# Optimization experiments

Measured on AMD Instinct MI355X. Metric: run time of the kernel, lower is better.

Reference implementation:

```python
import math
import jax, jax.numpy as jnp
import numpy as np


def setup_inputs() -> dict:
    key = jax.random.key(0)
    k1, k2 = jax.random.split(key)
    N, C, K = 1024, 4096, 16384
    x = jax.random.normal(k1, (N, C), dtype=jnp.float32)
    # xavier_normal for (C, K): std = sqrt(2/(C+K))
    w_std = math.sqrt(2.0 / (C + K))
    weights = jax.random.normal(k2, (C, K), dtype=jnp.float32) * w_std
    std = jnp.float32(10.0)
    return {"x": x, "weights": weights, "std": std}


def reference(x, weights, std):
    # x: (N, C); weights: (C, K)
    N, C = x.shape
    K = weights.shape[1]
    side = int(math.sqrt(K))

    # Squared distances ||w_k - x_n||^2 via expansion (same math as
    # norm(weights[None] - x[..., None], dim=1)**2, without the (N,C,K) tensor)
    x2 = jnp.sum(x * x, axis=1, keepdims=True)            # (N, 1)
    w2 = jnp.sum(weights * weights, axis=0)[None, :]       # (1, K)
    xw = jnp.einsum('nc,ck->nk', x, weights)               # (N, K) GEMM
    norms2 = jnp.maximum(x2 + w2 - 2.0 * xw, 0.0)          # (N, K)

    # Best matching unit (detached in original)
    bmu = jnp.argmin(norms2, axis=-1)                      # (N,) int

    # 2D radial basis over the side x side grid, centered at BMU
    row = (bmu // side).astype(jnp.float32)
    col = (bmu % side).astype(jnp.float32)
    t = jnp.arange(side, dtype=jnp.float32)
    gi, gj = jnp.meshgrid(t, t, indexing='ij')
    grid = jnp.stack([gi.reshape(-1), gj.reshape(-1)], axis=-1)  # (K, 2)
    pt = jnp.stack([row, col], axis=-1)[:, None, :]              # (N, 1, 2)
    d2 = jnp.sum((grid[None] - pt) ** 2, axis=-1)                # (N, K)
    phi = jnp.exp(-0.5 * d2 / (std ** 2))
    phi = phi / jnp.sum(phi, axis=-1, keepdims=True)

    return norms2 * phi
```

## Files before the change

### kernel.cpp

```cpp
#include <hip/hip_runtime.h>
#include <stdint.h>

#define NROWS 1024
#define CDIM  4096
#define KDIM  16384
#define SIDE  128

typedef __attribute__((ext_vector_type(8))) short short8;
typedef __attribute__((ext_vector_type(4))) float f32x4;

static __device__ __forceinline__ unsigned short f2bf(float f) {
  unsigned u = __float_as_uint(f);
  u += 0x7fffu + ((u >> 16) & 1u);
  return (unsigned short)(u >> 16);
}
static __device__ __forceinline__ float bf2f(unsigned short h) {
  return __uint_as_float(((unsigned)h) << 16);
}

#define GLOAD_LDS16(g, l)                                                     \
  __builtin_amdgcn_global_load_lds(                                           \
      (const __attribute__((address_space(1))) void*)(g),                     \
      (__attribute__((address_space(3))) void*)(l), 16, 0, 0)

#define SWZ(o) ((o) ^ (((o) >> 3) & 0x70))

__global__ void k_zero(float* __restrict__ w2) {
  w2[blockIdx.x * 256 + threadIdx.x] = 0.f;
}

__global__ __launch_bounds__(256) void k_wconv(const float* __restrict__ w,
                                               unsigned short* __restrict__ whT,
                                               unsigned short* __restrict__ wlT,
                                               float* __restrict__ w2) {
  __shared__ float T[64][65];
  const int k0 = blockIdx.x * 64, c0 = blockIdx.y * 64;
  const int t = threadIdx.x;
#pragma unroll
  for (int i = 0; i < 4; i++) {
    int e = i * 1024 + t * 4;
    int cr = e >> 6, kc = e & 63;
    float4 v = *(const float4*)(w + (size_t)(c0 + cr) * KDIM + k0 + kc);
    T[cr][kc] = v.x; T[cr][kc + 1] = v.y; T[cr][kc + 2] = v.z; T[cr][kc + 3] = v.w;
  }
  __syncthreads();
#pragma unroll
  for (int i = 0; i < 4; i++) {
    int e = i * 1024 + t * 4;
    int kr = e >> 6, cc = e & 63;
    ushort4 hv, lv;
    float f0 = T[cc + 0][kr], f1 = T[cc + 1][kr];
    float f2 = T[cc + 2][kr], f3 = T[cc + 3][kr];
    hv.x = f2bf(f0); lv.x = f2bf(f0 - bf2f(hv.x));
    hv.y = f2bf(f1); lv.y = f2bf(f1 - bf2f(hv.y));
    hv.z = f2bf(f2); lv.z = f2bf(f2 - bf2f(hv.z));
    hv.w = f2bf(f3); lv.w = f2bf(f3 - bf2f(hv.w));
    size_t off = (size_t)(k0 + kr) * CDIM + c0 + cc;
    *(ushort4*)(whT + off) = hv;
    *(ushort4*)(wlT + off) = lv;
    float s = f0 * f0 + f1 * f1 + f2 * f2 + f3 * f3;
#pragma unroll
    for (int off2 = 8; off2 > 0; off2 >>= 1) s += __shfl_down(s, off2);
    if ((t & 15) == 0) atomicAdd(&w2[k0 + kr], s);
  }
}

__global__ __launch_bounds__(256) void k_xconv(const float* __restrict__ x,
                                               unsigned short* __restrict__ xh) {
  size_t i = ((size_t)blockIdx.x * 256 + threadIdx.x) * 4;
  float4 v = *(const float4*)(x + i);
  ushort4 hv;
  hv.x = f2bf(v.x); hv.y = f2bf(v.y); hv.z = f2bf(v.z); hv.w = f2bf(v.w);
  *(ushort4*)(xh + i) = hv;
}

__global__ void k_x2(const float* __restrict__ x, float* __restrict__ x2) {
  const int n = blockIdx.x, l = threadIdx.x;
  const float* row = x + (size_t)n * CDIM;
  float s = 0.f;
#pragma unroll 4
  for (int i = 0; i < 16; i++) {
    float4 v = *(const float4*)(row + (i * 64 + l) * 4);
    s += v.x * v.x + v.y * v.y + v.z * v.z + v.w * v.w;
  }
#pragma unroll
  for (int off = 32; off > 0; off >>= 1) s += __shfl_down(s, off);
  if (l == 0) x2[n] = s;
}

__global__ __launch_bounds__(512, 2) void k_gemm(
    const unsigned short* __restrict__ xh,
    const unsigned short* __restrict__ whT,
    const float* __restrict__ x2, const float* __restrict__ w2,
    float* __restrict__ out) {
  extern __shared__ char smem[];
  const int t = threadIdx.x;
  const int b = blockIdx.x;
  const int L = (b & 7) * 32 + (b >> 3);
  const int m0 = (L & 3) * 256, n0 = (L >> 2) * 256;
  const int lane = t & 63, wid = t >> 6;
  const int wrow = (wid >> 2) * 128;
  const int wcol = (wid & 3) * 64;

  int rowS[4], cbS[4];
  uint32_t loffS[4];
#pragma unroll
  for (int i = 0; i < 4; i++) {
    int o_lin = (i * 512 + t) * 16;
    int o_log = SWZ(o_lin);
    rowS[i] = o_log >> 7;
    cbS[i] = (o_log & 127) >> 1;
    loffS[i] = i * 8192 + wid * 1024;
  }

  f32x4 acc[8][4];
#pragma unroll
  for (int m = 0; m < 8; m++)
#pragma unroll
    for (int n = 0; n < 4; n++) acc[m][n] = (f32x4){0.f, 0.f, 0.f, 0.f};

  const int rlo = lane & 15;
  const int kgb = (lane >> 4) * 16;

#define STAGE_TILE(tt, d)                                                     \
  {                                                                           \
    const int c0s = (tt) * 64;                                                \
    char* const dst = smem + (d) * 65536;                                     \
    _Pragma("unroll")                                                         \
    for (int i = 0; i < 4; i++) {                                             \
      size_t ga = (size_t)(m0 + rowS[i]) * CDIM + c0s + cbS[i];               \
      GLOAD_LDS16(xh + ga, dst + loffS[i]);                                   \
    }                                                                         \
    _Pragma("unroll")                                                         \
    for (int i = 0; i < 4; i++) {                                             \
      size_t gb = (size_t)(n0 + rowS[i]) * CDIM + c0s + cbS[i];               \
      GLOAD_LDS16(whT + gb, dst + 32768 + loffS[i]);                          \
    }                                                                         \
  }

  STAGE_TILE(0, 0);

  for (int tl = 0; tl < 64; ++tl) {
    const int cur = tl & 1;
    if (tl < 63) {
      STAGE_TILE(tl + 1, cur ^ 1);
      asm volatile("s_waitcnt vmcnt(8)" ::: "memory");
    } else {
      asm volatile("s_waitcnt vmcnt(0)" ::: "memory");
    }
    asm volatile("s_barrier" ::: "memory");

    const char* const Ab = smem + cur * 65536;
    const char* const Bb = Ab + 32768;
    short8 b_f[4][2];
#pragma unroll
    for (int n = 0; n < 4; n++)
#pragma unroll
      for (int ks = 0; ks < 2; ks++)
        b_f[n][ks] = *(const short8*)(Bb + SWZ((wcol + n * 16 + rlo) * 128 + ks * 64 + kgb));
    __builtin_amdgcn_s_setprio(1);
#pragma unroll
    for (int m = 0; m < 8; m++) {
      const char* ar = Ab + (wrow + m * 16 + rlo) * 128;
      short8 a0 = *(const short8*)(Ab + SWZ((wrow + m * 16 + rlo) * 128 + kgb));
      short8 a1 = *(const short8*)(Ab + SWZ((wrow + m * 16 + rlo) * 128 + 64 + kgb));
      (void)ar;
#pragma unroll
      for (int n = 0; n < 4; n++) {
        acc[m][n] = __builtin_amdgcn_mfma_f32_16x16x32_bf16(a0, b_f[n][0], acc[m][n], 0, 0, 0);
        acc[m][n] = __builtin_amdgcn_mfma_f32_16x16x32_bf16(a1, b_f[n][1], acc[m][n], 0, 0, 0);
      }
    }
    __builtin_amdgcn_s_setprio(0);
    asm volatile("s_barrier" ::: "memory");
  }
#undef STAGE_TILE

  float w2v[4];
#pragma unroll
  for (int n = 0; n < 4; n++) w2v[n] = w2[n0 + wcol + n * 16 + rlo];
#pragma unroll
  for (int m = 0; m < 8; m++) {
#pragma unroll
    for (int j = 0; j < 4; j++) {
      int row = m0 + wrow + m * 16 + (lane >> 4) * 4 + j;
      float xr = x2[row];
      float* orow = out + (size_t)row * KDIM;
#pragma unroll
      for (int n = 0; n < 4; n++) {
        int col = n0 + wcol + n * 16 + rlo;
        float v = xr + w2v[n] - 2.0f * acc[m][n][j];
        orow[col] = v < 0.f ? 0.f : v;
      }
    }
  }
}

__global__ __launch_bounds__(256) void k_fb(const float* __restrict__ x,
                                            const float* __restrict__ w,
                                            float* __restrict__ out) {
  __shared__ float xs[16][65];
  __shared__ float wsm[16][65];
  const int t = threadIdx.x;
  const int n0 = blockIdx.x * 64, k0 = blockIdx.y * 64;
  const int tx = t & 15, ty = t >> 4;
  float acc[4][4];
#pragma unroll
  for (int a = 0; a < 4; a++)
#pragma unroll
    for (int b = 0; b < 4; b++) acc[a][b] = 0.f;
  for (int c0 = 0; c0 < CDIM; c0 += 16) {
#pragma unroll
    for (int i = 0; i < 4; i++) {
      int e = i * 256 + t;
      int nl = e >> 4, cl = e & 15;
      xs[cl][nl] = x[(size_t)(n0 + nl) * CDIM + c0 + cl];
    }
#pragma unroll
    for (int i = 0; i < 4; i++) {
      int e = i * 256 + t;
      int cl = e >> 6, kl = e & 63;
      wsm[cl][kl] = w[(size_t)(c0 + cl) * KDIM + k0 + kl];
    }
    __syncthreads();
#pragma unroll
    for (int c = 0; c < 16; c++)
#pragma unroll
      for (int a = 0; a < 4; a++) {
        float xa = xs[c][ty * 4 + a];
#pragma unroll
        for (int b = 0; b < 4; b++) {
          float d = wsm[c][tx * 4 + b] - xa;
          acc[a][b] += d * d;
        }
      }
    __syncthreads();
  }
#pragma unroll
  for (int a = 0; a < 4; a++)
#pragma unroll
    for (int b = 0; b < 4; b++)
      out[(size_t)(n0 + ty * 4 + a) * KDIM + k0 + tx * 4 + b] = acc[a][b];
}

__global__ __launch_bounds__(256) void k_row(
    float* __restrict__ out, const float* __restrict__ stdp,
    const float* __restrict__ x, const unsigned short* __restrict__ whT,
    const unsigned short* __restrict__ wlT, const float* __restrict__ w2) {
  const int n = blockIdx.x, t = threadIdx.x;
  __shared__ alignas(16) float er[SIDE];
  __shared__ alignas(16) float ec[SIDE];
  __shared__ float rv[4];
  __shared__ float s_red[4];
  __shared__ int cand[128];
  __shared__ int s_ncand;
  __shared__ int s_bmu;
  __shared__ float s_inv;
  float* row = out + (size_t)n * KDIM;

  float bv = 3.4e38f;
#pragma unroll 4
  for (int i = 0; i < 16; i++) {
    float4 v = *(const float4*)(row + (t + i * 256) * 4);
    bv = fminf(fminf(fminf(bv, v.x), fminf(v.y, v.z)), v.w);
  }
#pragma unroll
  for (int off = 32; off > 0; off >>= 1) bv = fminf(bv, __shfl_down(bv, off));
  if ((t & 63) == 0) rv[t >> 6] = bv;
  if (t == 0) s_ncand = 0;
  __syncthreads();
  const float thr = fminf(fminf(rv[0], rv[1]), fminf(rv[2], rv[3])) + 0.05f;

#pragma unroll 4
  for (int i = 0; i < 16; i++) {
    int k = (t + i * 256) * 4;
    float4 v = *(const float4*)(row + k);
    if (v.x <= thr) { int j = atomicAdd(&s_ncand, 1); if (j < 128) cand[j] = k; }
    if (v.y <= thr) { int j = atomicAdd(&s_ncand, 1); if (j < 128) cand[j] = k + 1; }
    if (v.z <= thr) { int j = atomicAdd(&s_ncand, 1); if (j < 128) cand[j] = k + 2; }
    if (v.w <= thr) { int j = atomicAdd(&s_ncand, 1); if (j < 128) cand[j] = k + 3; }
  }
  __syncthreads();
  int nc = s_ncand < 128 ? s_ncand : 128;

  float best = 3.4e38f;
  int bestk = 0x7fffffff;
  const float* xr = x + (size_t)n * CDIM;
  for (int j = 0; j < nc; j++) {
    const int k = cand[j];
    const unsigned short* wh = whT + (size_t)k * CDIM;
    const unsigned short* wl = wlT + (size_t)k * CDIM;
    float s = 0.f;
#pragma unroll
    for (int ii = 0; ii < 2; ii++) {
      int c = (ii * 256 + t) * 8;
      short8 h8 = *(const short8*)(wh + c);
      short8 l8 = *(const short8*)(wl + c);
      float4 xa = *(const float4*)(xr + c);
      float4 xb = *(const float4*)(xr + c + 4);
      s += xa.x * (bf2f((unsigned short)h8[0]) + bf2f((unsigned short)l8[0]));
      s += xa.y * (bf2f((unsigned short)h8[1]) + bf2f((unsigned short)l8[1]));
      s += xa.z * (bf2f((unsigned short)h8[2]) + bf2f((unsigned short)l8[2]));
      s += xa.w * (bf2f((unsigned short)h8[3]) + bf2f((unsigned short)l8[3]));
      s += xb.x * (bf2f((unsigned short)h8[4]) + bf2f((unsigned short)l8[4]));
      s += xb.y * (bf2f((unsigned short)h8[5]) + bf2f((unsigned short)l8[5]));
      s += xb.z * (bf2f((unsigned short)h8[6]) + bf2f((unsigned short)l8[6]));
      s += xb.w * (bf2f((unsigned short)h8[7]) + bf2f((unsigned short)l8[7]));
    }
#pragma unroll
    for (int off = 32; off > 0; off >>= 1) s += __shfl_down(s, off);
    if ((t & 63) == 0) s_red[t >> 6] = s;
    __syncthreads();
    if (t == 0) {
      float dot = s_red[0] + s_red[1] + s_red[2] + s_red[3];
      float sc = w2[k] - 2.0f * dot;
      if (sc < best || (sc == best && k < bestk)) { best = sc; bestk = k; }
    }
    __syncthreads();
  }
  if (t == 0) s_bmu = bestk;
  __syncthreads();

  const int bmu = s_bmu;
  const float sd = stdp[0];
  const float inv2s2 = -0.5f / (sd * sd);
  const float rr = (float)(bmu >> 7), ccol = (float)(bmu & 127);
  if (t < 128) {
    float d = (float)t - rr;
    er[t] = expf(d * d * inv2s2);
  } else {
    int j = t - 128;
    float d = (float)j - ccol;
    ec[j] = expf(d * d * inv2s2);
  }
  __syncthreads();
  if (t == 0) {
    float Sr = 0.f, Sc = 0.f;
    for (int i = 0; i < SIDE; i++) { Sr += er[i]; Sc += ec[i]; }
    s_inv = 1.0f / (Sr * Sc);
  }
  __syncthreads();
  const float inv = s_inv;
#pragma unroll 4
  for (int i = 0; i < 16; i++) {
    int k = (t + i * 256) * 4;
    float4 v = *(const float4*)(row + k);
    float e_r = er[k >> 7] * inv;
    const float4 e4 = *(const float4*)(&ec[k & 127]);
    v.x *= e_r * e4.x;
    v.y *= e_r * e4.y;
    v.z *= e_r * e4.z;
    v.w *= e_r * e4.w;
    *(float4*)(row + k) = v;
  }
}

__global__ __launch_bounds__(256) void k_row_fb(float* __restrict__ out,
                                                const float* __restrict__ stdp) {
  const int n = blockIdx.x, t = threadIdx.x;
  __shared__ alignas(16) float er[SIDE];
  __shared__ alignas(16) float ec[SIDE];
  __shared__ float rv[4];
  __shared__ int ri[4];
  __shared__ float s_inv;
  __shared__ int s_bmu;
  float* row = out + (size_t)n * KDIM;

  float bv = 3.4e38f;
  int bi = 0;
#pragma unroll 4
  for (int i = 0; i < 16; i++) {
    int k = (t + i * 256) * 4;
    float4 v = *(const float4*)(row + k);
    if (v.x < bv) { bv = v.x; bi = k; }
    if (v.y < bv) { bv = v.y; bi = k + 1; }
    if (v.z < bv) { bv = v.z; bi = k + 2; }
    if (v.w < bv) { bv = v.w; bi = k + 3; }
  }
#pragma unroll
  for (int off = 32; off > 0; off >>= 1) {
    float ov = __shfl_down(bv, off);
    int oi = __shfl_down(bi, off);
    if (ov < bv || (ov == bv && oi < bi)) { bv = ov; bi = oi; }
  }
  if ((t & 63) == 0) { rv[t >> 6] = bv; ri[t >> 6] = bi; }
  __syncthreads();
  if (t == 0) {
    for (int i = 1; i < 4; i++)
      if (rv[i] < bv || (rv[i] == bv && ri[i] < bi)) { bv = rv[i]; bi = ri[i]; }
    s_bmu = bi;
  }
  __syncthreads();
  const int bmu = s_bmu;
  const float sd = stdp[0];
  const float inv2s2 = -0.5f / (sd * sd);
  const float rr = (float)(bmu >> 7), ccol = (float)(bmu & 127);
  if (t < 128) {
    float d = (float)t - rr;
    er[t] = expf(d * d * inv2s2);
  } else {
    int j = t - 128;
    float d = (float)j - ccol;
    ec[j] = expf(d * d * inv2s2);
  }
  __syncthreads();
  if (t == 0) {
    float Sr = 0.f, Sc = 0.f;
    for (int i = 0; i < SIDE; i++) { Sr += er[i]; Sc += ec[i]; }
    s_inv = 1.0f / (Sr * Sc);
  }
  __syncthreads();
  const float inv = s_inv;
#pragma unroll 4
  for (int i = 0; i < 16; i++) {
    int k = (t + i * 256) * 4;
    float4 v = *(const float4*)(row + k);
    float e_r = er[k >> 7] * inv;
    const float4 e4 = *(const float4*)(&ec[k & 127]);
    v.x *= e_r * e4.x;
    v.y *= e_r * e4.y;
    v.z *= e_r * e4.z;
    v.w *= e_r * e4.w;
    *(float4*)(row + k) = v;
  }
}

extern "C" void kernel_launch(void* const* d_in, const int* in_sizes, int n_in,
                              void* d_out, int out_size, void* d_ws, size_t ws_size,
                              hipStream_t stream) {
  (void)in_sizes; (void)n_in; (void)out_size;
  const float* x = (const float*)d_in[0];
  const float* w = (const float*)d_in[1];
  const float* stdp = (const float*)d_in[2];
  float* out = (float*)d_out;

  const size_t sz_wT = (size_t)KDIM * CDIM * sizeof(unsigned short);
  const size_t sz_x  = (size_t)NROWS * CDIM * sizeof(unsigned short);
  const size_t need = 2 * sz_wT + sz_x + (size_t)NROWS * 4 + (size_t)KDIM * 4;

  if (ws_size >= need) {
    char* p = (char*)d_ws;
    unsigned short* whT = (unsigned short*)p; p += sz_wT;
    unsigned short* wlT = (unsigned short*)p; p += sz_wT;
    unsigned short* xh  = (unsigned short*)p; p += sz_x;
    float* x2 = (float*)p; p += (size_t)NROWS * 4;
    float* w2 = (float*)p;

    static int lds_ok = -1;
    if (lds_ok < 0)
      lds_ok = (int)hipFuncSetAttribute((const void*)k_gemm,
                                        hipFuncAttributeMaxDynamicSharedMemorySize,
                                        131072);

    k_zero<<<KDIM / 256, 256, 0, stream>>>(w2);
    k_wconv<<<dim3(KDIM / 64, CDIM / 64), 256, 0, stream>>>(w, whT, wlT, w2);
    k_xconv<<<(NROWS * CDIM) / 1024, 256, 0, stream>>>(x, xh);
    k_x2<<<NROWS, 64, 0, stream>>>(x, x2);
    k_gemm<<<256, 512, 131072, stream>>>(xh, whT, x2, w2, out);
    k_row<<<NROWS, 256, 0, stream>>>(out, stdp, x, whT, wlT, w2);
  } else {
    k_fb<<<dim3(NROWS / 64, KDIM / 64), 256, 0, stream>>>(x, w, out);
    k_row_fb<<<NROWS, 256, 0, stream>>>(out, stdp);
  }
}
```

Before: 293.2 us.

## Split GEMM K-tile into half-stages interleaving global-to-LDS loads with MFMA clusters

Measured after the change: 298.9 us. About the same (+1.9%).

```diff
diff --git a/kernel.cpp b/kernel.cpp
--- a/kernel.cpp
+++ b/kernel.cpp
@@ -22,8 +22,6 @@
   __builtin_amdgcn_global_load_lds(                                           \
       (const __attribute__((address_space(1))) void*)(g),                     \
       (__attribute__((address_space(3))) void*)(l), 16, 0, 0)
-
-#define SWZ(o) ((o) ^ (((o) >> 3) & 0x70))
 
 __global__ void k_zero(float* __restrict__ w2) {
   w2[blockIdx.x * 256 + threadIdx.x] = 0.f;
@@ -101,17 +99,15 @@
   const int lane = t & 63, wid = t >> 6;
   const int wrow = (wid >> 2) * 128;
   const int wcol = (wid & 3) * 64;
-
-  int rowS[4], cbS[4];
-  uint32_t loffS[4];
-#pragma unroll
-  for (int i = 0; i < 4; i++) {
-    int o_lin = (i * 512 + t) * 16;
-    int o_log = SWZ(o_lin);
-    rowS[i] = o_log >> 7;
-    cbS[i] = (o_log & 127) >> 1;
-    loffS[i] = i * 8192 + wid * 1024;
-  }
+  const int rlo = lane & 15;
+  const int kg16 = (lane >> 4) * 16;
+
+  const int rS = t >> 2;
+  const int cbS = (t & 3) * 8;
+  const uint32_t ldst = (uint32_t)wid * 1024;
+
+  const uint32_t aRB = (uint32_t)(wrow + rlo) * 64 + kg16;
+  const uint32_t bRB = 32768u + (uint32_t)(wcol + rlo) * 64 + kg16;
 
   f32x4 acc[8][4];
 #pragma unroll
@@ -119,62 +115,84 @@
 #pragma unroll
     for (int n = 0; n < 4; n++) acc[m][n] = (f32x4){0.f, 0.f, 0.f, 0.f};
 
-  const int rlo = lane & 15;
-  const int kgb = (lane >> 4) * 16;
-
-#define STAGE_TILE(tt, d)                                                     \
-  {                                                                           \
-    const int c0s = (tt) * 64;                                                \
-    char* const dst = smem + (d) * 65536;                                     \
+#define STAGE_HALF(tt, S)                                                     \
+  do {                                                                        \
+    if ((tt) < 64) {                                                          \
+      char* dst = smem + ((tt) & 1) * 65536 + (S) * 16384;                    \
+      const unsigned short* gb = ((S) >= 2 ? whT : xh);                       \
+      const int gr0 = ((S) >= 2 ? n0 : m0);                                   \
+      const int gc0 = (tt) * 64 + ((S) & 1) * 32;                             \
+      _Pragma("unroll")                                                       \
+      for (int i_ = 0; i_ < 2; i_++) {                                        \
+        size_t g = (size_t)(gr0 + i_ * 128 + rS) * CDIM + gc0 + cbS;          \
+        GLOAD_LDS16(gb + g, dst + i_ * 8192 + ldst);                          \
+      }                                                                       \
+    }                                                                         \
+  } while (0)
+
+#define DO_MFMA(mh)                                                           \
+  do {                                                                        \
+    __builtin_amdgcn_s_barrier();                                             \
+    asm volatile("s_waitcnt lgkmcnt(0)" ::: "memory");                        \
+    __builtin_amdgcn_sched_barrier(0);                                        \
+    __builtin_amdgcn_s_setprio(1);                                            \
     _Pragma("unroll")                                                         \
-    for (int i = 0; i < 4; i++) {                                             \
-      size_t ga = (size_t)(m0 + rowS[i]) * CDIM + c0s + cbS[i];               \
-      GLOAD_LDS16(xh + ga, dst + loffS[i]);                                   \
-    }                                                                         \
-    _Pragma("unroll")                                                         \
-    for (int i = 0; i < 4; i++) {                                             \
-      size_t gb = (size_t)(n0 + rowS[i]) * CDIM + c0s + cbS[i];               \
-      GLOAD_LDS16(whT + gb, dst + 32768 + loffS[i]);                          \
-    }                                                                         \
-  }
-
-  STAGE_TILE(0, 0);
+    for (int m_ = 0; m_ < 4; m_++)                                            \
+      _Pragma("unroll")                                                       \
+      for (int n_ = 0; n_ < 4; n_++)                                          \
+        acc[(mh) * 4 + m_][n_] = __builtin_amdgcn_mfma_f32_16x16x32_bf16(     \
+            af[m_], bf[n_], acc[(mh) * 4 + m_][n_], 0, 0, 0);                 \
+    __builtin_amdgcn_s_setprio(0);                                            \
+    __builtin_amdgcn_s_barrier();                                             \
+  } while (0)
+
+  STAGE_HALF(0, 0);
+  STAGE_HALF(0, 2);
+  STAGE_HALF(0, 1);
+  STAGE_HALF(0, 3);
+  asm volatile("s_waitcnt vmcnt(0)" ::: "memory");
+  __builtin_amdgcn_s_barrier();
 
   for (int tl = 0; tl < 64; ++tl) {
-    const int cur = tl & 1;
+    const uint32_t dbase = (uint32_t)(tl & 1) * 65536;
+    short8 af[4], bf[4];
+#pragma unroll
+    for (int n = 0; n < 4; n++)
+      bf[n] = *(const short8*)(smem + dbase + bRB + n * 1024);
+#pragma unroll
+    for (int m = 0; m < 4; m++)
+      af[m] = *(const short8*)(smem + dbase + aRB + m * 1024);
+    STAGE_HALF(tl + 1, 0);
+    DO_MFMA(0);
+#pragma unroll
+    for (int m = 0; m < 4; m++)
+      af[m] = *(const short8*)(smem + dbase + aRB + (m + 4) * 1024);
+    STAGE_HALF(tl + 1, 2);
     if (tl < 63) {
-      STAGE_TILE(tl + 1, cur ^ 1);
-      asm volatile("s_waitcnt vmcnt(8)" ::: "memory");
+      asm volatile("s_waitcnt vmcnt(4)" ::: "memory");
     } else {
       asm volatile("s_waitcnt vmcnt(0)" ::: "memory");
     }
-    asm volatile("s_barrier" ::: "memory");
-
-    const char* const Ab = smem + cur * 65536;
-    const char* const Bb = Ab + 32768;
-    short8 b_f[4][2];
+    DO_MFMA(1);
 #pragma unroll
     for (int n = 0; n < 4; n++)
-#pragma unroll
-      for (int ks = 0; ks < 2; ks++)
-        b_f[n][ks] = *(const short8*)(Bb + SWZ((wcol + n * 16 + rlo) * 128 + ks * 64 + kgb));
-    __builtin_amdgcn_s_setprio(1);
-#pragma unroll
-    for (int m = 0; m < 8; m++) {
-      const char* ar = Ab + (wrow + m * 16 + rlo) * 128;
-      short8 a0 = *(const short8*)(Ab + SWZ((wrow + m * 16 + rlo) * 128 + kgb));
-      short8 a1 = *(const short8*)(Ab + SWZ((wrow + m * 16 + rlo) * 128 + 64 + kgb));
-      (void)ar;
-#pragma unroll
-      for (int n = 0; n < 4; n++) {
-        acc[m][n] = __builtin_amdgcn_mfma_f32_16x16x32_bf16(a0, b_f[n][0], acc[m][n], 0, 0, 0);
-        acc[m][n] = __builtin_amdgcn_mfma_f32_16x16x32_bf16(a1, b_f[n][1], acc[m][n], 0, 0, 0);
-      }
-    }
-    __builtin_amdgcn_s_setprio(0);
-    asm volatile("s_barrier" ::: "memory");
-  }
-#undef STAGE_TILE
+      bf[n] = *(const short8*)(smem + dbase + 16384 + bRB + n * 1024);
+#pragma unroll
+    for (int m = 0; m < 4; m++)
+      af[m] = *(const short8*)(smem + dbase + 16384 + aRB + m * 1024);
+    STAGE_HALF(tl + 1, 1);
+    DO_MFMA(0);
+#pragma unroll
+    for (int m = 0; m < 4; m++)
+      af[m] = *(const short8*)(smem + dbase + 16384 + aRB + (m + 4) * 1024);
+    STAGE_HALF(tl + 1, 3);
+    if (tl < 63) {
+      asm volatile("s_waitcnt vmcnt(4)" ::: "memory");
+    }
+    DO_MFMA(1);
+  }
+#undef STAGE_HALF
+#undef DO_MFMA
 
   float w2v[4];
 #pragma unroll
```

## Split GEMM K-tile into quarter-stage loads interleaved with MFMA phases

Applied to the files above, without the earlier changes.

Measured after the change: 321.4 us. +9.6%, slower.

```diff
diff --git a/kernel.cpp b/kernel.cpp
--- a/kernel.cpp
+++ b/kernel.cpp
@@ -101,17 +101,20 @@
   const int lane = t & 63, wid = t >> 6;
   const int wrow = (wid >> 2) * 128;
   const int wcol = (wid & 3) * 64;
-
-  int rowS[4], cbS[4];
-  uint32_t loffS[4];
-#pragma unroll
-  for (int i = 0; i < 4; i++) {
-    int o_lin = (i * 512 + t) * 16;
-    int o_log = SWZ(o_lin);
-    rowS[i] = o_log >> 7;
-    cbS[i] = (o_log & 127) >> 1;
-    loffS[i] = i * 8192 + wid * 1024;
-  }
+  const int rlo = lane & 15;
+  const int kg16 = (lane >> 4) * 16;
+
+  int rowH[2][2], colH[2][2];
+#pragma unroll
+  for (int h = 0; h < 2; h++)
+#pragma unroll
+    for (int j = 0; j < 2; j++) {
+      uint32_t o_full = (uint32_t)h * 16384u + (uint32_t)j * 8192u +
+                        (uint32_t)wid * 1024u + (uint32_t)lane * 16u;
+      uint32_t o_log = SWZ(o_full);
+      rowH[h][j] = (int)(o_log >> 7);
+      colH[h][j] = (int)((o_log & 127) >> 1);
+    }
 
   f32x4 acc[8][4];
 #pragma unroll
@@ -119,62 +122,94 @@
 #pragma unroll
     for (int n = 0; n < 4; n++) acc[m][n] = (f32x4){0.f, 0.f, 0.f, 0.f};
 
-  const int rlo = lane & 15;
-  const int kgb = (lane >> 4) * 16;
-
-#define STAGE_TILE(tt, d)                                                     \
-  {                                                                           \
-    const int c0s = (tt) * 64;                                                \
-    char* const dst = smem + (d) * 65536;                                     \
+#define STAGE_HALF(tt, S)                                                     \
+  do {                                                                        \
+    const int tc_ = (tt) < 63 ? (tt) : 63;     \
+    char* dst_ = smem + (((tt) & 1) * 65536) + (S) * 16384;                   \
+    const unsigned short* gp_ = ((S) >= 2) ? whT : xh;                        \
+    const int gr0_ = ((S) >= 2) ? n0 : m0;                                    \
+    const int h_ = (S) & 1;                                                   \
+    const int c0s_ = tc_ * 64;                                                \
     _Pragma("unroll")                                                         \
-    for (int i = 0; i < 4; i++) {                                             \
-      size_t ga = (size_t)(m0 + rowS[i]) * CDIM + c0s + cbS[i];               \
-      GLOAD_LDS16(xh + ga, dst + loffS[i]);                                   \
+    for (int j_ = 0; j_ < 2; j_++) {                                          \
+      size_t g_ = (size_t)(gr0_ + rowH[h_][j_]) * CDIM + c0s_ + colH[h_][j_]; \
+      GLOAD_LDS16(gp_ + g_, dst_ + j_ * 8192 + wid * 1024);                   \
     }                                                                         \
-    _Pragma("unroll")                                                         \
-    for (int i = 0; i < 4; i++) {                                             \
-      size_t gb = (size_t)(n0 + rowS[i]) * CDIM + c0s + cbS[i];               \
-      GLOAD_LDS16(whT + gb, dst + 32768 + loffS[i]);                          \
-    }                                                                         \
-  }
-
-  STAGE_TILE(0, 0);
+  } while (0)
+
+  STAGE_HALF(0, 0); STAGE_HALF(0, 2); STAGE_HALF(0, 1); STAGE_HALF(0, 3);
+  STAGE_HALF(1, 0); STAGE_HALF(1, 2); STAGE_HALF(1, 1);
+  asm volatile("s_waitcnt vmcnt(6)" ::: "memory");
+  __builtin_amdgcn_s_barrier();
 
   for (int tl = 0; tl < 64; ++tl) {
-    const int cur = tl & 1;
-    if (tl < 63) {
-      STAGE_TILE(tl + 1, cur ^ 1);
-      asm volatile("s_waitcnt vmcnt(8)" ::: "memory");
-    } else {
-      asm volatile("s_waitcnt vmcnt(0)" ::: "memory");
-    }
-    asm volatile("s_barrier" ::: "memory");
-
-    const char* const Ab = smem + cur * 65536;
+    const char* const Ab = smem + (tl & 1) * 65536;
     const char* const Bb = Ab + 32768;
-    short8 b_f[4][2];
+    short8 a0[8], b0[4], a1[8], b1[4];
+
 #pragma unroll
     for (int n = 0; n < 4; n++)
-#pragma unroll
-      for (int ks = 0; ks < 2; ks++)
-        b_f[n][ks] = *(const short8*)(Bb + SWZ((wcol + n * 16 + rlo) * 128 + ks * 64 + kgb));
+      b0[n] = *(const short8*)(Bb + SWZ((wcol + n * 16 + rlo) * 128 + kg16));
+#pragma unroll
+    for (int m = 0; m < 8; m++)
+      a0[m] = *(const short8*)(Ab + SWZ((wrow + m * 16 + rlo) * 128 + kg16));
+    __builtin_amdgcn_s_barrier();
+    asm volatile("s_waitcnt lgkmcnt(0)" ::: "memory");
+    __builtin_amdgcn_sched_barrier(0);
     __builtin_amdgcn_s_setprio(1);
 #pragma unroll
-    for (int m = 0; m < 8; m++) {
-      const char* ar = Ab + (wrow + m * 16 + rlo) * 128;
-      short8 a0 = *(const short8*)(Ab + SWZ((wrow + m * 16 + rlo) * 128 + kgb));
-      short8 a1 = *(const short8*)(Ab + SWZ((wrow + m * 16 + rlo) * 128 + 64 + kgb));
-      (void)ar;
-#pragma unroll
-      for (int n = 0; n < 4; n++) {
-        acc[m][n] = __builtin_amdgcn_mfma_f32_16x16x32_bf16(a0, b_f[n][0], acc[m][n], 0, 0, 0);
-        acc[m][n] = __builtin_amdgcn_mfma_f32_16x16x32_bf16(a1, b_f[n][1], acc[m][n], 0, 0, 0);
-      }
-    }
+    for (int m = 0; m < 4; m++)
+#pragma unroll
+      for (int n = 0; n < 4; n++)
+        acc[m][n] = __builtin_amdgcn_mfma_f32_16x16x32_bf16(a0[m], b0[n], acc[m][n], 0, 0, 0);
     __builtin_amdgcn_s_setprio(0);
-    asm volatile("s_barrier" ::: "memory");
-  }
-#undef STAGE_TILE
+    __builtin_amdgcn_s_barrier();
+
+#pragma unroll
+    for (int n = 0; n < 4; n++)
+      b1[n] = *(const short8*)(Bb + SWZ((wcol + n * 16 + rlo) * 128 + 64 + kg16));
+#pragma unroll
+    for (int m = 0; m < 8; m++)
+      a1[m] = *(const short8*)(Ab + SWZ((wrow + m * 16 + rlo) * 128 + 64 + kg16));
+    STAGE_HALF(tl + 1, 3);
+    __builtin_amdgcn_s_barrier();
+    asm volatile("s_waitcnt lgkmcnt(0)" ::: "memory");
+    __builtin_amdgcn_sched_barrier(0);
+    __builtin_amdgcn_s_setprio(1);
+#pragma unroll
+    for (int m = 4; m < 8; m++)
+#pragma unroll
+      for (int n = 0; n < 4; n++)
+        acc[m][n] = __builtin_amdgcn_mfma_f32_16x16x32_bf16(a0[m], b0[n], acc[m][n], 0, 0, 0);
+    __builtin_amdgcn_s_setprio(0);
+    __builtin_amdgcn_s_barrier();
+
+    STAGE_HALF(tl + 2, 0);
+    STAGE_HALF(tl + 2, 2);
+    asm volatile("s_waitcnt vmcnt(6)" ::: "memory");
+    __builtin_amdgcn_s_barrier();
+    __builtin_amdgcn_s_setprio(1);
+#pragma unroll
+    for (int m = 0; m < 4; m++)
+#pragma unroll
+      for (int n = 0; n < 4; n++)
+        acc[m][n] = __builtin_amdgcn_mfma_f32_16x16x32_bf16(a1[m], b1[n], acc[m][n], 0, 0, 0);
+    __builtin_amdgcn_s_setprio(0);
+    __builtin_amdgcn_s_barrier();
+
+    STAGE_HALF(tl + 2, 1);
+    asm volatile("s_waitcnt vmcnt(6)" ::: "memory");
+    __builtin_amdgcn_s_barrier();
+    __builtin_amdgcn_s_setprio(1);
+#pragma unroll
+    for (int m = 4; m < 8; m++)
+#pragma unroll
+      for (int n = 0; n < 4; n++)
+        acc[m][n] = __builtin_amdgcn_mfma_f32_16x16x32_bf16(a1[m], b1[n], acc[m][n], 0, 0, 0);
+    __builtin_amdgcn_s_setprio(0);
+    __builtin_amdgcn_s_barrier();
+  }
+#undef STAGE_HALF
 
   float w2v[4];
 #pragma unroll
```

## Fuse row-min into GEMM epilogue and switch to 32x32x16 MFMA

Applied to the files above, without the earlier changes.

Measured after the change: 382.7 us. 1.31x slower.

```diff
diff --git a/kernel.cpp b/kernel.cpp
--- a/kernel.cpp
+++ b/kernel.cpp
@@ -8,6 +8,7 @@
 
 typedef __attribute__((ext_vector_type(8))) short short8;
 typedef __attribute__((ext_vector_type(4))) float f32x4;
+typedef __attribute__((ext_vector_type(16))) float f32x16;
 
 static __device__ __forceinline__ unsigned short f2bf(float f) {
   unsigned u = __float_as_uint(f);
@@ -25,8 +26,10 @@
 
 #define SWZ(o) ((o) ^ (((o) >> 3) & 0x70))
 
-__global__ void k_zero(float* __restrict__ w2) {
-  w2[blockIdx.x * 256 + threadIdx.x] = 0.f;
+__global__ void k_zero(float* __restrict__ w2, unsigned* __restrict__ rowmin) {
+  int i = blockIdx.x * 256 + threadIdx.x;
+  w2[i] = 0.f;
+  if (i < NROWS) rowmin[i] = 0x7f7fffffu;
 }
 
 __global__ __launch_bounds__(256) void k_wconv(const float* __restrict__ w,
@@ -92,7 +95,7 @@
     const unsigned short* __restrict__ xh,
     const unsigned short* __restrict__ whT,
     const float* __restrict__ x2, const float* __restrict__ w2,
-    float* __restrict__ out) {
+    float* __restrict__ out, unsigned* __restrict__ rowmin) {
   extern __shared__ char smem[];
   const int t = threadIdx.x;
   const int b = blockIdx.x;
@@ -101,6 +104,9 @@
   const int lane = t & 63, wid = t >> 6;
   const int wrow = (wid >> 2) * 128;
   const int wcol = (wid & 3) * 64;
+  const int r31 = lane & 31;
+  const int hk = lane >> 5;
+  const int hk16 = hk * 16;
 
   int rowS[4], cbS[4];
   uint32_t loffS[4];
@@ -113,14 +119,13 @@
     loffS[i] = i * 8192 + wid * 1024;
   }
 
-  f32x4 acc[8][4];
-#pragma unroll
-  for (int m = 0; m < 8; m++)
-#pragma unroll
-    for (int n = 0; n < 4; n++) acc[m][n] = (f32x4){0.f, 0.f, 0.f, 0.f};
-
-  const int rlo = lane & 15;
-  const int kgb = (lane >> 4) * 16;
+  f32x16 acc[4][2];
+#pragma unroll
+  for (int m = 0; m < 4; m++)
+#pragma unroll
+    for (int n = 0; n < 2; n++)
+#pragma unroll
+      for (int q = 0; q < 16; q++) acc[m][n][q] = 0.f;
 
 #define STAGE_TILE(tt, d)                                                     \
   {                                                                           \
@@ -152,23 +157,17 @@
 
     const char* const Ab = smem + cur * 65536;
     const char* const Bb = Ab + 32768;
-    short8 b_f[4][2];
-#pragma unroll
-    for (int n = 0; n < 4; n++)
-#pragma unroll
-      for (int ks = 0; ks < 2; ks++)
-        b_f[n][ks] = *(const short8*)(Bb + SWZ((wcol + n * 16 + rlo) * 128 + ks * 64 + kgb));
     __builtin_amdgcn_s_setprio(1);
 #pragma unroll
-    for (int m = 0; m < 8; m++) {
-      const char* ar = Ab + (wrow + m * 16 + rlo) * 128;
-      short8 a0 = *(const short8*)(Ab + SWZ((wrow + m * 16 + rlo) * 128 + kgb));
-      short8 a1 = *(const short8*)(Ab + SWZ((wrow + m * 16 + rlo) * 128 + 64 + kgb));
-      (void)ar;
-#pragma unroll
-      for (int n = 0; n < 4; n++) {
-        acc[m][n] = __builtin_amdgcn_mfma_f32_16x16x32_bf16(a0, b_f[n][0], acc[m][n], 0, 0, 0);
-        acc[m][n] = __builtin_amdgcn_mfma_f32_16x16x32_bf16(a1, b_f[n][1], acc[m][n], 0, 0, 0);
+    for (int ks = 0; ks < 4; ks++) {
+      const int kb = ks * 32 + hk16;
+      short8 b0 = *(const short8*)(Bb + SWZ((wcol + r31) * 128 + kb));
+      short8 b1 = *(const short8*)(Bb + SWZ((wcol + 32 + r31) * 128 + kb));
+#pragma unroll
+      for (int m = 0; m < 4; m++) {
+        short8 am = *(const short8*)(Ab + SWZ((wrow + m * 32 + r31) * 128 + kb));
+        acc[m][0] = __builtin_amdgcn_mfma_f32_32x32x16_bf16(am, b0, acc[m][0], 0, 0, 0);
+        acc[m][1] = __builtin_amdgcn_mfma_f32_32x32x16_bf16(am, b1, acc[m][1], 0, 0, 0);
       }
     }
     __builtin_amdgcn_s_setprio(0);
@@ -176,22 +175,25 @@
   }
 #undef STAGE_TILE
 
-  float w2v[4];
-#pragma unroll
-  for (int n = 0; n < 4; n++) w2v[n] = w2[n0 + wcol + n * 16 + rlo];
-#pragma unroll
-  for (int m = 0; m < 8; m++) {
-#pragma unroll
-    for (int j = 0; j < 4; j++) {
-      int row = m0 + wrow + m * 16 + (lane >> 4) * 4 + j;
+  const float w2v0 = w2[n0 + wcol + r31];
+  const float w2v1 = w2[n0 + wcol + 32 + r31];
+#pragma unroll
+  for (int m = 0; m < 4; m++) {
+#pragma unroll
+    for (int reg = 0; reg < 16; reg++) {
+      int row = m0 + wrow + m * 32 + (reg & 3) + 8 * (reg >> 2) + 4 * hk;
       float xr = x2[row];
       float* orow = out + (size_t)row * KDIM;
-#pragma unroll
-      for (int n = 0; n < 4; n++) {
-        int col = n0 + wcol + n * 16 + rlo;
-        float v = xr + w2v[n] - 2.0f * acc[m][n][j];
-        orow[col] = v < 0.f ? 0.f : v;
-      }
+      float v0 = xr + w2v0 - 2.0f * acc[m][0][reg];
+      float v1 = xr + w2v1 - 2.0f * acc[m][1][reg];
+      v0 = v0 < 0.f ? 0.f : v0;
+      v1 = v1 < 0.f ? 0.f : v1;
+      orow[n0 + wcol + r31] = v0;
+      orow[n0 + wcol + 32 + r31] = v1;
+      float vm = fminf(v0, v1);
+#pragma unroll
+      for (int msk = 1; msk <= 16; msk <<= 1) vm = fminf(vm, __shfl_xor(vm, msk));
+      if (r31 == 0) atomicMin(&rowmin[row], __float_as_uint(vm));
     }
   }
 }
@@ -246,11 +248,11 @@
 __global__ __launch_bounds__(256) void k_row(
     float* __restrict__ out, const float* __restrict__ stdp,
     const float* __restrict__ x, const unsigned short* __restrict__ whT,
-    const unsigned short* __restrict__ wlT, const float* __restrict__ w2) {
+    const unsigned short* __restrict__ wlT, const float* __restrict__ w2,
+    const unsigned* __restrict__ rowmin) {
   const int n = blockIdx.x, t = threadIdx.x;
   __shared__ alignas(16) float er[SIDE];
   __shared__ alignas(16) float ec[SIDE];
-  __shared__ float rv[4];
   __shared__ float s_red[4];
   __shared__ int cand[128];
   __shared__ int s_ncand;
@@ -258,18 +260,9 @@
   __shared__ float s_inv;
   float* row = out + (size_t)n * KDIM;
 
-  float bv = 3.4e38f;
-#pragma unroll 4
-  for (int i = 0; i < 16; i++) {
-    float4 v = *(const float4*)(row + (t + i * 256) * 4);
-    bv = fminf(fminf(fminf(bv, v.x), fminf(v.y, v.z)), v.w);
-  }
-#pragma unroll
-  for (int off = 32; off > 0; off >>= 1) bv = fminf(bv, __shfl_down(bv, off));
-  if ((t & 63) == 0) rv[t >> 6] = bv;
   if (t == 0) s_ncand = 0;
   __syncthreads();
-  const float thr = fminf(fminf(rv[0], rv[1]), fminf(rv[2], rv[3])) + 0.05f;
+  const float thr = __uint_as_float(rowmin[n]) + 0.05f;
 
 #pragma unroll 4
   for (int i = 0; i < 16; i++) {
@@ -436,7 +429,8 @@
 
   const size_t sz_wT = (size_t)KDIM * CDIM * sizeof(unsigned short);
   const size_t sz_x  = (size_t)NROWS * CDIM * sizeof(unsigned short);
-  const size_t need = 2 * sz_wT + sz_x + (size_t)NROWS * 4 + (size_t)KDIM * 4;
+  const size_t need = 2 * sz_wT + sz_x + (size_t)NROWS * 4 + (size_t)KDIM * 4 +
+                      (size_t)NROWS * 4;
 
   if (ws_size >= need) {
     char* p = (char*)d_ws;
@@ -444,7 +438,8 @@
     unsigned short* wlT = (unsigned short*)p; p += sz_wT;
     unsigned short* xh  = (unsigned short*)p; p += sz_x;
     float* x2 = (float*)p; p += (size_t)NROWS * 4;
-    float* w2 = (float*)p;
+    float* w2 = (float*)p; p += (size_t)KDIM * 4;
+    unsigned* rowmin = (unsigned*)p;
 
     static int lds_ok = -1;
     if (lds_ok < 0)
@@ -452,12 +447,12 @@
                                         hipFuncAttributeMaxDynamicSharedMemorySize,
                                         131072);
 
-    k_zero<<<KDIM / 256, 256, 0, stream>>>(w2);
+    k_zero<<<KDIM / 256, 256, 0, stream>>>(w2, rowmin);
     k_wconv<<<dim3(KDIM / 64, CDIM / 64), 256, 0, stream>>>(w, whT, wlT, w2);
     k_xconv<<<(NROWS * CDIM) / 1024, 256, 0, stream>>>(x, xh);
     k_x2<<<NROWS, 64, 0, stream>>>(x, x2);
-    k_gemm<<<256, 512, 131072, stream>>>(xh, whT, x2, w2, out);
-    k_row<<<NROWS, 256, 0, stream>>>(out, stdp, x, whT, wlT, w2);
+    k_gemm<<<256, 512, 131072, stream>>>(xh, whT, x2, w2, out, rowmin);
+    k_row<<<NROWS, 256, 0, stream>>>(out, stdp, x, whT, wlT, w2, rowmin);
   } else {
     k_fb<<<dim3(NROWS / 64, KDIM / 64), 256, 0, stream>>>(x, w, out);
     k_row_fb<<<NROWS, 256, 0, stream>>>(out, stdp);
```
